# Optimization experiments

Measured on AMD Instinct MI355X. Metric: run time of the kernel, lower is better.

Reference implementation:

```python
import jax, jax.numpy as jnp
import numpy as np

OSF = 15.0  # over_sample_factor
EXPMAX = 50.0
AFROMZERO = 0.02
AFROMC = 0.01


def zmax_calc(a, b, c=1.0):
    # a is a scalar, b (= b*mT^2) is per-element, c == 1.0
    a_is_zero = a < AFROMZERO
    a_is_c = jnp.abs(a - c) < AFROMC
    z_zero = jnp.where(c > b, b / c, 1.0)
    z_c = b / (b + c)
    denom = jnp.where(a_is_c, 1.0, c - a)  # safe denom; branch masked below
    z_gen = 0.5 * (b + c - jnp.sqrt((b - c) ** 2 + 4.0 * a * b)) / denom
    z_gen = jnp.where((z_gen > 0.9999) & (b > 100.0), jnp.minimum(z_gen, 1.0 - a / b), z_gen)
    return jnp.where(a_is_zero, z_zero, jnp.where(a_is_c, z_c, z_gen))


def likelihood(z, mT, a, b):
    # Lund fragmentation f(z) ratio kernel, c = 1.0
    b_exp = b * mT ** 2
    z_max = zmax_calc(a, b_exp, 1.0)
    f_exp = b_exp * (1.0 / z_max - 1.0 / z) + jnp.log(z_max / z)
    a_coef = a * jnp.log((1.0 - z) / (1.0 - z_max))
    f_exp = f_exp + jnp.where(a < AFROMZERO, 0.0, a_coef)
    return jnp.exp(jnp.clip(f_exp, -EXPMAX, EXPMAX))


def setup_inputs() -> dict:
    key = jax.random.key(0)
    kz, kr, km, kmult, kdrop, kzero = jax.random.split(key, 6)
    B, M, R = 8192, 128, 24  # batch, max multiplicity, reject slots
    mult = jax.random.randint(kmult, (B,), 20, M + 1)  # event multiplicities
    valid = jnp.arange(M)[None, :] < mult[:, None]  # [B, M]

    z_acc = jax.random.uniform(kz, (B, M), minval=0.05, maxval=0.95)
    z_acc = jnp.where(valid & (jax.random.uniform(kzero, (B, M)) > 0.1), z_acc, 0.0)

    z_rej = jax.random.uniform(kr, (B, M, R), minval=0.05, maxval=0.95)
    keep = jax.random.uniform(kdrop, (B, M, R)) < 0.4  # ragged # of rejections
    z_rej = jnp.where(valid[:, :, None] & keep, z_rej, 0.0)

    z = jnp.concatenate([z_acc[:, :, None], z_rej], axis=2).astype(jnp.float32)
    mT = jax.random.uniform(km, (B, M), minval=0.2, maxval=2.0, dtype=jnp.float32)
    observable = jnp.stack([mult, jnp.zeros_like(mult)], axis=1).astype(jnp.int64)

    return {
        "z": z,
        "mT": mT,
        "observable": observable,
        "params_a": jnp.float32(0.72),
        "params_b": jnp.float32(1.05),
        "params_base": jnp.array([0.68, 0.98], dtype=jnp.float32),
    }


def reference(z, mT, observable, params_a, params_b, params_base):
    B, M, _ = z.shape
    mult = observable[:, 0]
    valid = jnp.arange(M)[None, :] < mult[:, None]  # [B, M]
    a0, b0 = params_base[0], params_base[1]

    # accepted z's (column 0)
    z_acc = z[:, :, 0]
    m_acc = (z_acc != 0.0) & valid
    zs = jnp.where(m_acc, z_acc, 0.5)  # safe fill for masked slots
    mTs = jnp.where(m_acc, mT, 1.0)
    w_acc = likelihood(zs, mTs, params_a, params_b) / likelihood(zs, mTs, a0, b0)
    w_acc = jnp.where(m_acc, w_acc, 1.0)

    # rejected z's (columns 1:), each row j uses mT[i, j]
    z_rej = z[:, :, 1:]
    m_rej = (z_rej != 0.0) & valid[:, :, None]
    zr = jnp.where(m_rej, z_rej, 0.5)
    mTr = jnp.where(m_rej, mT[:, :, None], 1.0)
    w_rej = (OSF - likelihood(zr, mTr, params_a, params_b)) / (
        OSF - likelihood(zr, mTr, a0, b0))
    w_rej = jnp.where(m_rej, w_rej, 1.0)

    return jnp.prod(w_acc, axis=1) * jnp.prod(w_rej, axis=(1, 2))
```

## Files before the change

### kernel.cpp

```cpp
#include <hip/hip_runtime.h>

#define AFROMZERO 0.02f
#define AFROMC    0.01f
#define OSF       15.0f
#define LOG2E     1.4426950408889634f
#define EXPMAX2   (50.0f * LOG2E)

__device__ __forceinline__ float zmax_calc(float a, float b) {
    if (a < AFROMZERO) return fminf(b, 1.0f);
    if (fabsf(a - 1.0f) < AFROMC) return b / (b + 1.0f);
    float d  = (b - 1.0f) * (b - 1.0f) + 4.0f * a * b;
    float zg = 0.5f * (b + 1.0f - sqrtf(d)) / (1.0f - a);
    if (zg > 0.9999f && b > 100.0f) zg = fminf(zg, 1.0f - a / b);
    return zg;
}

__device__ __forceinline__ void set_consts2(float a, float b, float mTv,
                                            float& C2, float& be2) {
    float be = b * mTv * mTv;
    float zm = zmax_calc(a, be);
    be2 = be * LOG2E;
    float c = be2 / zm + log2f(zm);
    if (a >= AFROMZERO) c -= a * log2f(1.0f - zm);
    C2 = c;
}

__global__ __launch_bounds__(256) void lund_weight_kernel(
    const float* __restrict__ z,
    const float* __restrict__ mT,
    const int*   __restrict__ obs,
    const float* __restrict__ pa_p,
    const float* __restrict__ pb_p,
    const float* __restrict__ base_p,
    float* __restrict__ out)
{
    __shared__ float s_part[4];

    const int tid  = threadIdx.x;
    const int r0   = blockIdx.x * 2;
    const int half = tid >> 7;
    const int m    = tid & 127;
    const int row  = r0 + half;
    const int mult = obs[2 * row];
    const bool live = m < mult;

    float v[25];
    {
        const float* gp = z + (size_t)row * 3200 + m * 25;
        if (live) {
            #pragma unroll
            for (int c = 0; c < 6; ++c)
                __builtin_memcpy(&v[4 * c], gp + 4 * c, 16);
            v[24] = gp[24];
        }
    }

    const float pa = pa_p[0], pb = pb_p[0];
    const float a0 = base_p[0], b0 = base_p[1];
    const float an = (pa < AFROMZERO) ? 0.0f : pa;
    const float ao = (a0 < AFROMZERO) ? 0.0f : a0;

    const float mTv = mT[(size_t)row * 128 + m];
    float Cn2, ben2, Co2, beo2;
    set_consts2(pa, pb, mTv, Cn2, ben2);
    set_consts2(a0, b0, mTv, Co2, beo2);

    float w = 1.0f;
    if (live) {
        float facN = 1.0f, facD = 1.0f;
        #pragma unroll
        for (int k = 0; k < 25; ++k) {
            float zz  = v[k];
            bool  act = (zz != 0.0f);
            float zs  = act ? zz : 0.5f;
            float rz  = __builtin_amdgcn_rcpf(zs);
            float lz  = __builtin_amdgcn_logf(zs);
            float l1  = __builtin_amdgcn_logf(1.0f - zs);
            float fn  = fmaf(-ben2, rz, Cn2) + fmaf(an, l1, -lz);
            float fo  = fmaf(-beo2, rz, Co2) + fmaf(ao, l1, -lz);
            fn = fminf(fmaxf(fn, -EXPMAX2), EXPMAX2);
            fo = fminf(fmaxf(fo, -EXPMAX2), EXPMAX2);
            float Ln = __builtin_amdgcn_exp2f(fn);
            float Lo = __builtin_amdgcn_exp2f(fo);
            float fN = (k == 0) ? Ln : (OSF - Ln);
            float fD = (k == 0) ? Lo : (OSF - Lo);
            facN *= act ? fN : 1.0f;
            facD *= act ? fD : 1.0f;
        }
        w = facN / facD;
    }

    for (int mask = 1; mask < 64; mask <<= 1)
        w *= __shfl_xor(w, mask, 64);
    if ((tid & 63) == 0) s_part[tid >> 6] = w;
    __syncthreads();
    if (tid == 0)   out[r0]     = s_part[0] * s_part[1];
    if (tid == 128) out[r0 + 1] = s_part[2] * s_part[3];
}

extern "C" void kernel_launch(void* const* d_in, const int* in_sizes, int n_in,
                              void* d_out, int out_size, void* d_ws, size_t ws_size,
                              hipStream_t stream) {
    const float* z    = (const float*)d_in[0];
    const float* mT   = (const float*)d_in[1];
    const int*   obs  = (const int*)d_in[2];
    const float* pa   = (const float*)d_in[3];
    const float* pb   = (const float*)d_in[4];
    const float* base = (const float*)d_in[5];
    float* out = (float*)d_out;

    int B = in_sizes[0] / (128 * 25);
    lund_weight_kernel<<<B / 2, 256, 0, stream>>>(z, mT, obs, pa, pb, base, out);
}
```

Measured before the change: 158.2 us.

## Stage z rows into LDS with coalesced global_load_lds per wave

Replaces the per-thread strided 100-byte loads of z with wave-cooperative 16-byte direct-to-LDS loads (global_load_lds), so each wave reads its contiguous 64×25 chunk fully coalesced. Threads then read their 25 values from LDS. It also sizes the copy to the live element count, skipping dead slots. This costs 28 KB of LDS per block, which may limit occupancy, and LDS reads with stride 25 may cause bank conflicts.

```diff
diff --git a/kernel.cpp b/kernel.cpp
--- a/kernel.cpp
+++ b/kernel.cpp
@@ -25,6 +25,9 @@
     C2 = c;
 }
 
+typedef const __attribute__((address_space(1))) void* as1_cvp;
+typedef __attribute__((address_space(3))) void* as3_vp;
+
 __global__ __launch_bounds__(256) void lund_weight_kernel(
     const float* __restrict__ z,
     const float* __restrict__ mT,
@@ -34,25 +37,31 @@
     const float* __restrict__ base_p,
     float* __restrict__ out)
 {
+    __shared__ float s_z[4 * 1792];
     __shared__ float s_part[4];
 
-    const int tid  = threadIdx.x;
-    const int r0   = blockIdx.x * 2;
-    const int half = tid >> 7;
-    const int m    = tid & 127;
-    const int row  = r0 + half;
+    const int tid   = threadIdx.x;
+    const int lane  = tid & 63;
+    const int wv    = tid >> 6;
+    const int r0    = blockIdx.x * 2;
+    const int half  = wv >> 1;
+    const int mbase = (wv & 1) << 6;
+    const int row   = r0 + half;
+    const int m     = mbase + lane;
+
     const int mult = obs[2 * row];
-    const bool live = m < mult;
+    const int cnt  = min(max(mult - mbase, 0), 64);
+    const int nch  = (cnt * 25 + 255) >> 8;
 
-    float v[25];
-    {
-        const float* gp = z + (size_t)row * 3200 + m * 25;
-        if (live) {
-            #pragma unroll
-            for (int c = 0; c < 6; ++c)
-                __builtin_memcpy(&v[4 * c], gp + 4 * c, 16);
-            v[24] = gp[24];
-        }
+    float*       sw = s_z + wv * 1792;
+    const float* gw = z + (size_t)row * 3200 + mbase * 25;
+
+    for (int c = 0; c < nch; ++c) {
+        const int off = (c << 8) + (lane << 2);
+        const float* gp = gw + off;
+        if (off >= 1600) gp = gw;
+        __builtin_amdgcn_global_load_lds((as1_cvp)gp, (as3_vp)(sw + (c << 8)),
+                                         16, 0, 0);
     }
 
     const float pa = pa_p[0], pb = pb_p[0];
@@ -65,12 +74,15 @@
     set_consts2(pa, pb, mTv, Cn2, ben2);
     set_consts2(a0, b0, mTv, Co2, beo2);
 
+    asm volatile("s_waitcnt vmcnt(0)" ::: "memory");
+
     float w = 1.0f;
-    if (live) {
+    if (lane < cnt) {
+        const float* zp = sw + lane * 25;
         float facN = 1.0f, facD = 1.0f;
         #pragma unroll
         for (int k = 0; k < 25; ++k) {
-            float zz  = v[k];
+            float zz  = zp[k];
             bool  act = (zz != 0.0f);
             float zs  = act ? zz : 0.5f;
             float rz  = __builtin_amdgcn_rcpf(zs);
@@ -92,7 +104,7 @@
 
     for (int mask = 1; mask < 64; mask <<= 1)
         w *= __shfl_xor(w, mask, 64);
-    if ((tid & 63) == 0) s_part[tid >> 6] = w;
+    if (lane == 0) s_part[wv] = w;
     __syncthreads();
     if (tid == 0)   out[r0]     = s_part[0] * s_part[1];
     if (tid == 128) out[r0 + 1] = s_part[2] * s_part[3];
```

After: 158.8 us. Within noise of the previous version (+0.4%).
